# Kernel optimization log

Hardware: AMD Instinct MI355X
Metric: run time of the kernel (lower is better)

The kernel has to match this reference:

```python
import jax, jax.numpy as jnp
import numpy as np

B, NW = 1024, 300
N = NW // 3          # 100 tokens (keypoints)
E = 5                # token dim after cat of PE(2): 3 + 2
H, D, L = 4, 64, 3   # heads, d_attention, layers


def setup_inputs() -> dict:
    key = jax.random.key(0)
    ks = jax.random.split(key, 8)
    s = jnp.float32(0.1)
    x = jax.random.normal(ks[0], (B, NW), dtype=jnp.float32)
    Wq = jax.random.normal(ks[1], (L, H, D, E), dtype=jnp.float32) * s  # per-head W_Q (no bias)
    Wk = jax.random.normal(ks[2], (L, H, D, E), dtype=jnp.float32) * s
    Wv = jax.random.normal(ks[3], (L, H, D, E), dtype=jnp.float32) * s
    Wo = jax.random.normal(ks[4], (L, E, H * D), dtype=jnp.float32) * s  # MHA output proj (no bias)
    Wf = jax.random.normal(ks[5], (L, E, E), dtype=jnp.float32) * s      # FFN linear
    bf = jax.random.normal(ks[6], (L, E), dtype=jnp.float32) * s
    g1 = jnp.ones((L, E), dtype=jnp.float32)
    b1 = jnp.zeros((L, E), dtype=jnp.float32)
    g2 = jnp.ones((L, E), dtype=jnp.float32)
    b2 = jnp.zeros((L, E), dtype=jnp.float32)
    return dict(x=x, Wq=Wq, Wk=Wk, Wv=Wv, Wo=Wo, Wf=Wf, bf=bf,
                g1=g1, b1=b1, g2=g2, b2=b2)


def _layer_norm(x, g, b, eps=1e-5):
    mu = jnp.mean(x, axis=-1, keepdims=True)
    var = jnp.mean((x - mu) ** 2, axis=-1, keepdims=True)  # biased, like torch LN
    return (x - mu) / jnp.sqrt(var + eps) * g + b


def reference(x, Wq, Wk, Wv, Wo, Wf, bf, g1, b1, g2, b2):
    kp = x.reshape(B, N, 3)                      # 'b (n d) -> b n d', d=3
    mask = kp[:, :, -1] > 0                      # [B,N] keypoint confidence mask
    # PositionalEncoding(d_model=2, kind='cat'): div_term=[1] -> pe=[sin(pos),cos(pos)]
    pos = jnp.arange(N, dtype=jnp.float32)
    pe = jnp.stack([jnp.sin(pos), jnp.cos(pos)], axis=-1)         # [N,2]
    out = jnp.concatenate([kp, jnp.broadcast_to(pe, (B, N, 2))], axis=-1)  # [B,N,5]
    out = jnp.where(mask[:, :, None], out, jnp.float32(0.0))      # out[~mask]=0

    pair = mask[:, None, None, :] & mask[:, None, :, None]        # [B,1,N,N]
    neg = -jnp.finfo(jnp.float32).max
    scale = jnp.float32(1.0 / np.sqrt(D))
    for l in range(L):
        # per-head projections (heads vectorized over h)
        q = jnp.einsum('bne,hde->bhnd', out, Wq[l])
        k = jnp.einsum('bne,hde->bhnd', out, Wk[l])
        v = jnp.einsum('bne,hde->bhnd', out, Wv[l])
        dots = jnp.einsum('bhid,bhjd->bhij', q, k) * scale        # [B,H,N,N]
        dots = jnp.where(pair, dots, neg)
        attn = jax.nn.softmax(dots, axis=-1)
        o = jnp.einsum('bhij,bhjd->bhid', attn, v)                # [B,H,N,D]
        o = o.transpose(0, 2, 1, 3).reshape(B, N, H * D)          # concat heads
        attn_out = o @ Wo[l].T                                    # [B,N,E]
        ln1 = _layer_norm(attn_out + out, g1[l], b1[l])
        ffn = jax.nn.relu(ln1 @ Wf[l].T + bf[l])
        out = _layer_norm(ffn + ln1, g2[l], b2[l])
    return out
```

## Files before the change

### kernel.cpp

```cpp
#include <hip/hip_runtime.h>
#include <math.h>

#define NTOK 100
#define EDIM 5
#define NH   4
#define NL   3
#define DD   64
#define BLK  256

__global__ void precompute_mp(const float* __restrict__ Wq,
                              const float* __restrict__ Wk,
                              const float* __restrict__ Wv,
                              const float* __restrict__ Wo,
                              float* __restrict__ mp) {
  const int blk = blockIdx.x;
  const int which = blk / 12;
  const int rem = blk % 12;
  const int l = rem / 4, h = rem % 4;
  const int t = threadIdx.x;

  __shared__ float A[320];
  __shared__ float Bsh[320];

  const float* wa = (which ? Wv : Wq) + (l*NH + h)*DD*EDIM;
  for (int r = t; r < 320; r += 64) A[r] = wa[r];
  if (which == 0) {
    const float* wk = Wk + (l*NH + h)*DD*EDIM;
    for (int r = t; r < 320; r += 64) Bsh[r] = wk[r];
  } else {
    for (int r = t; r < 320; r += 64) {
      int f = r >> 6, d = r & 63;
      Bsh[r] = Wo[(l*EDIM + f)*(NH*DD) + h*DD + d];
    }
  }
  __syncthreads();
  if (t < 25) {
    int e = t / 5, f = t % 5;
    float acc = 0.f;
    if (which == 0) {
      #pragma unroll 8
      for (int d = 0; d < DD; ++d) acc += A[d*5+e] * Bsh[d*5+f];
      acc *= 0.125f * 1.44269504088896340736f;
    } else {
      #pragma unroll 8
      for (int d = 0; d < DD; ++d) acc += A[d*5+e] * Bsh[f*64+d];
    }
    mp[which*960 + ((l*NH + h)*EDIM + e)*8 + f] = acc;
  }
}

__global__ __launch_bounds__(BLK, 4) void encoder_kernel(
    const float* __restrict__ x,
    const float* __restrict__ mp,
    const float* __restrict__ Wf,
    const float* __restrict__ bfv,
    const float* __restrict__ g1,
    const float* __restrict__ b1,
    const float* __restrict__ g2,
    const float* __restrict__ b2,
    float* __restrict__ out)
{
  const int b = blockIdx.x, t = threadIdx.x;
  const int wv = t >> 6;
  const int ln = t & 63;

  __shared__ float4 s_MP4[480];
  __shared__ float4 s_o4[NH][NTOK+2];
  __shared__ float  s_o1[NH][NTOK+2];
  __shared__ float4 s_wp4[2][NH][NTOK+2];
  __shared__ float  s_wp1[2][NH][NTOK+2];
  __shared__ int    s_cidx[NTOK];
  __shared__ unsigned long long s_bal[2];

  const float* mpf = (const float*)s_MP4;
  for (int r = t; r < 480; r += BLK) s_MP4[r] = ((const float4*)mp)[r];

  float k0=0.f, k1=0.f, k2=0.f, msk=0.f;
  if (t < NTOK) {
    k0 = x[b*300 + 3*t];
    k1 = x[b*300 + 3*t + 1];
    k2 = x[b*300 + 3*t + 2];
    msk = (k2 > 0.f) ? 1.f : 0.f;
  }
  unsigned long long bal = __ballot(t < NTOK && msk != 0.f);
  if (t == 0)  s_bal[0] = bal;
  if (t == 64) s_bal[1] = bal;
  __syncthreads();
  const unsigned long long bw0 = s_bal[0], bw1 = s_bal[1];
  const int nm = __popcll(bw0) + __popcll(bw1);
  if (t < NTOK) {
    int lane = t & 63;
    unsigned long long lm = (lane == 0) ? 0ull : ((1ull << lane) - 1ull);
    int pre = (t < 64) ? __popcll(bw0 & lm) : (__popcll(bw0) + __popcll(bw1 & lm));
    if (msk != 0.f) {
      float4 v = make_float4(k0, k1, k2, sinf((float)t));
      float v4 = cosf((float)t);
      #pragma unroll
      for (int w = 0; w < NH; ++w) { s_o4[w][pre] = v; s_o1[w][pre] = v4; }
      s_cidx[t] = pre;
    } else {
      s_cidx[t] = nm;
    }
  }
  if (t == 0) {
    #pragma unroll
    for (int w = 0; w < NH; ++w) {
      s_o4[w][nm] = make_float4(0.f,0.f,0.f,0.f);
      s_o1[w][nm] = 0.f;
    }
  }
  __syncthreads();

  const int rows = nm + 1;
  const int npass = (rows > 64) ? 2 : 1;
  const float4* ow4 = s_o4[wv];
  const float*  ow1 = s_o1[wv];
  int bufp = 0;

  for (int l = 0; l < NL; ++l) {
    const float* Mh = mpf + ((l*NH + wv)*EDIM)*8;
    const float* Ph = mpf + 960 + ((l*NH + wv)*EDIM)*8;

    for (int ps = 0; ps < npass; ++ps) {
      const int i = ln + (ps << 6);
      if (i < rows) {
        const bool rep = (i == nm);
        float4 ov = ow4[i]; float ov4 = ow1[i];
        float o_[5] = {ov.x, ov.y, ov.z, ov.w, ov4};
        float a0=0.f,a1=0.f,a2=0.f,a3=0.f,a4=0.f;
        #pragma unroll
        for (int e = 0; e < 5; ++e) {
          float4 mr = *(const float4*)(Mh + e*8); float m4 = Mh[e*8+4];
          a0 += o_[e]*mr.x; a1 += o_[e]*mr.y; a2 += o_[e]*mr.z;
          a3 += o_[e]*mr.w; a4 += o_[e]*m4;
        }
        if (rep) { a0=0.f; a1=0.f; a2=0.f; a3=0.f; a4=0.f; }

        float w0=0.f,w1=0.f,w2=0.f,w3=0.f,w4=0.f, ls=0.f;
        #pragma unroll 4
        for (int j = 0; j < nm; ++j) {
          float4 oj = ow4[j]; float oe = ow1[j];
          float s = a0*oj.x + a1*oj.y + a2*oj.z + a3*oj.w + a4*oe;
          float p = exp2f(s);
          ls += p;
          w0 += p*oj.x; w1 += p*oj.y; w2 += p*oj.z; w3 += p*oj.w; w4 += p*oe;
        }
        if (rep) {
          float wext = (float)(NTOK - nm);
          w0 += wext*o_[0]; w1 += wext*o_[1]; w2 += wext*o_[2];
          w3 += wext*o_[3]; w4 += wext*o_[4];
        }
        float inv = 1.f / (rep ? (float)NTOK : ls);
        float we[5] = {w0,w1,w2,w3,w4};
        float c0=0.f,c1=0.f,c2=0.f,c3=0.f,c4=0.f;
        #pragma unroll
        for (int e = 0; e < 5; ++e) {
          float4 pr = *(const float4*)(Ph + e*8); float p4 = Ph[e*8+4];
          c0 += we[e]*pr.x; c1 += we[e]*pr.y; c2 += we[e]*pr.z;
          c3 += we[e]*pr.w; c4 += we[e]*p4;
        }
        s_wp4[bufp][wv][i] = make_float4(c0*inv, c1*inv, c2*inv, c3*inv);
        s_wp1[bufp][wv][i] = c4*inv;
      }
    }
    __syncthreads();

    for (int ps = 0; ps < npass; ++ps) {
      const int i = ln + (ps << 6);
      if (i < rows) {
        float4 ov = ow4[i]; float ov4 = ow1[i];
        float y[5] = {ov.x, ov.y, ov.z, ov.w, ov4};
        #pragma unroll
        for (int hh = 0; hh < NH; ++hh) {
          float4 wa = s_wp4[bufp][hh][i];
          y[0] += wa.x; y[1] += wa.y; y[2] += wa.z; y[3] += wa.w;
          y[4] += s_wp1[bufp][hh][i];
        }
        float mu = 0.2f*(y[0]+y[1]+y[2]+y[3]+y[4]);
        float var = 0.f;
        #pragma unroll
        for (int e = 0; e < 5; ++e) { float d = y[e]-mu; var += d*d; }
        var *= 0.2f;
        float inv1 = 1.f / sqrtf(var + 1e-5f);
        float ln1[5];
        #pragma unroll
        for (int e = 0; e < 5; ++e) ln1[e] = (y[e]-mu)*inv1*g1[l*5+e] + b1[l*5+e];
        float r2[5];
        #pragma unroll
        for (int e = 0; e < 5; ++e) {
          float acc = bfv[l*5+e];
          #pragma unroll
          for (int f = 0; f < 5; ++f) acc += ln1[f]*Wf[(l*5+e)*5+f];
          acc = acc > 0.f ? acc : 0.f;
          r2[e] = acc + ln1[e];
        }
        float mu2 = 0.2f*(r2[0]+r2[1]+r2[2]+r2[3]+r2[4]);
        float var2 = 0.f;
        #pragma unroll
        for (int e = 0; e < 5; ++e) { float d = r2[e]-mu2; var2 += d*d; }
        var2 *= 0.2f;
        float inv2 = 1.f / sqrtf(var2 + 1e-5f);
        float no[5];
        #pragma unroll
        for (int e = 0; e < 5; ++e) no[e] = (r2[e]-mu2)*inv2*g2[l*5+e] + b2[l*5+e];
        s_o4[wv][i] = make_float4(no[0], no[1], no[2], no[3]);
        s_o1[wv][i] = no[4];
      }
    }
    bufp ^= 1;
  }
  __syncthreads();

  for (int r = t; r < NTOK*EDIM; r += BLK) {
    int i = r / EDIM;
    int e = r - i*EDIM;
    int c = s_cidx[i];
    float v = (e < 4) ? ((const float*)&s_o4[0][c])[e] : s_o1[0][c];
    out[b*(NTOK*EDIM) + r] = v;
  }
}

extern "C" void kernel_launch(void* const* d_in, const int* in_sizes, int n_in,
                              void* d_out, int out_size, void* d_ws, size_t ws_size,
                              hipStream_t stream) {
  const float* x  = (const float*)d_in[0];
  const float* Wq = (const float*)d_in[1];
  const float* Wk = (const float*)d_in[2];
  const float* Wv = (const float*)d_in[3];
  const float* Wo = (const float*)d_in[4];
  const float* Wf = (const float*)d_in[5];
  const float* bf = (const float*)d_in[6];
  const float* g1 = (const float*)d_in[7];
  const float* b1 = (const float*)d_in[8];
  const float* g2 = (const float*)d_in[9];
  const float* b2 = (const float*)d_in[10];
  float* outp = (float*)d_out;
  float* mp   = (float*)d_ws;

  precompute_mp<<<24, 64, 0, stream>>>(Wq, Wk, Wv, Wo, mp);
  encoder_kernel<<<1024, BLK, 0, stream>>>(x, mp, Wf, bf, g1, b1, g2, b2, outp);
}
```

Measured before the change: 138.9 us.

## Split key range across two waves per head and broadcast keys via readlane

Doubles the block to 512 threads so that each head gets two waves, and each wave handles half of the compacted key range. The partial exp-sums and weighted sums are merged in the update phase. Token states now stay in registers, and keys are broadcast with readlane instead of being re-read from shared memory per head. The change also uses the hardware exp2 and rcp intrinsics. It is meant to cut the serial per-lane key loop length and LDS traffic, at the cost of more threads per block, higher register pressure and an extra shared merge.

```diff
diff --git a/kernel.cpp b/kernel.cpp
--- a/kernel.cpp
+++ b/kernel.cpp
@@ -6,7 +6,19 @@
 #define NH   4
 #define NL   3
 #define DD   64
-#define BLK  256
+#define BLK  512
+
+#if __has_builtin(__builtin_amdgcn_exp2f)
+#define EXP2(x) __builtin_amdgcn_exp2f(x)
+#else
+#define EXP2(x) exp2f(x)
+#endif
+#if __has_builtin(__builtin_amdgcn_rcpf)
+#define RCPF(x) __builtin_amdgcn_rcpf(x)
+#else
+#define RCPF(x) (1.f/(x))
+#endif
+#define RL(v, l) __int_as_float(__builtin_amdgcn_readlane(__float_as_int(v), (l)))
 
 __global__ void precompute_mp(const float* __restrict__ Wq,
                               const float* __restrict__ Wk,
@@ -49,7 +61,7 @@
   }
 }
 
-__global__ __launch_bounds__(BLK, 4) void encoder_kernel(
+__global__ __launch_bounds__(BLK, 8) void encoder_kernel(
     const float* __restrict__ x,
     const float* __restrict__ mp,
     const float* __restrict__ Wf,
@@ -61,19 +73,20 @@
     float* __restrict__ out)
 {
   const int b = blockIdx.x, t = threadIdx.x;
-  const int wv = t >> 6;
-  const int ln = t & 63;
+  const int wv = t >> 6, ln = t & 63;
+  const int h = wv >> 1, g = wv & 1;
 
   __shared__ float4 s_MP4[480];
-  __shared__ float4 s_o4[NH][NTOK+2];
-  __shared__ float  s_o1[NH][NTOK+2];
-  __shared__ float4 s_wp4[2][NH][NTOK+2];
-  __shared__ float  s_wp1[2][NH][NTOK+2];
+  __shared__ float4 s_w4[NH][2][104];
+  __shared__ float2 s_w2[NH][2][104];
+  __shared__ float4 s_i4[104];
+  __shared__ float  s_i1[104];
   __shared__ int    s_cidx[NTOK];
   __shared__ unsigned long long s_bal[2];
 
   const float* mpf = (const float*)s_MP4;
   for (int r = t; r < 480; r += BLK) s_MP4[r] = ((const float4*)mp)[r];
+  for (int r = t; r < 104; r += BLK) { s_i4[r] = make_float4(0.f,0.f,0.f,0.f); s_i1[r] = 0.f; }
 
   float k0=0.f, k1=0.f, k2=0.f, msk=0.f;
   if (t < NTOK) {
@@ -93,129 +106,148 @@
     unsigned long long lm = (lane == 0) ? 0ull : ((1ull << lane) - 1ull);
     int pre = (t < 64) ? __popcll(bw0 & lm) : (__popcll(bw0) + __popcll(bw1 & lm));
     if (msk != 0.f) {
-      float4 v = make_float4(k0, k1, k2, sinf((float)t));
-      float v4 = cosf((float)t);
-      #pragma unroll
-      for (int w = 0; w < NH; ++w) { s_o4[w][pre] = v; s_o1[w][pre] = v4; }
+      s_i4[pre] = make_float4(k0, k1, k2, sinf((float)t));
+      s_i1[pre] = cosf((float)t);
       s_cidx[t] = pre;
     } else {
       s_cidx[t] = nm;
     }
   }
-  if (t == 0) {
-    #pragma unroll
-    for (int w = 0; w < NH; ++w) {
-      s_o4[w][nm] = make_float4(0.f,0.f,0.f,0.f);
-      s_o1[w][nm] = 0.f;
-    }
-  }
   __syncthreads();
 
   const int rows = nm + 1;
-  const int npass = (rows > 64) ? 2 : 1;
-  const float4* ow4 = s_o4[wv];
-  const float*  ow1 = s_o1[wv];
-  int bufp = 0;
+  const bool twoRows = (rows > 64);
+
+  float oA0,oA1,oA2,oA3,oA4, oB0,oB1,oB2,oB3,oB4;
+  { float4 v = s_i4[ln]; oA0=v.x; oA1=v.y; oA2=v.z; oA3=v.w; oA4=s_i1[ln]; }
+  if (ln < 40) { float4 v = s_i4[ln+64]; oB0=v.x; oB1=v.y; oB2=v.z; oB3=v.w; oB4=s_i1[ln+64]; }
+  else { oB0=0.f; oB1=0.f; oB2=0.f; oB3=0.f; oB4=0.f; }
+
+  const int jmid = nm >> 1;
+  const int jlo  = g ? jmid : 0;
+  const int jhi  = g ? nm : jmid;
+  const int jhiA = (jhi < 64) ? jhi : 64;
+  const int jloB = (jlo > 64) ? jlo : 64;
+  const float wext = (float)(NTOK - nm);
 
   for (int l = 0; l < NL; ++l) {
-    const float* Mh = mpf + ((l*NH + wv)*EDIM)*8;
-    const float* Ph = mpf + 960 + ((l*NH + wv)*EDIM)*8;
-
-    for (int ps = 0; ps < npass; ++ps) {
-      const int i = ln + (ps << 6);
-      if (i < rows) {
-        const bool rep = (i == nm);
-        float4 ov = ow4[i]; float ov4 = ow1[i];
-        float o_[5] = {ov.x, ov.y, ov.z, ov.w, ov4};
-        float a0=0.f,a1=0.f,a2=0.f,a3=0.f,a4=0.f;
+    const float* Mh = mpf + ((l*NH + h)*EDIM)*8;
+    const float* Ph = mpf + 960 + ((l*NH + h)*EDIM)*8;
+
+    auto attn_row = [&](float o0,float o1,float o2,float o3,float o4,int row) {
+      float oc[5] = {o0,o1,o2,o3,o4};
+      float a0=0.f,a1=0.f,a2=0.f,a3=0.f,a4=0.f;
+      #pragma unroll
+      for (int e = 0; e < 5; ++e) {
+        float4 mr = *(const float4*)(Mh + e*8); float m4 = Mh[e*8+4];
+        a0 += oc[e]*mr.x; a1 += oc[e]*mr.y; a2 += oc[e]*mr.z;
+        a3 += oc[e]*mr.w; a4 += oc[e]*m4;
+      }
+      const bool rep = (row == nm);
+      if (rep) { a0=0.f; a1=0.f; a2=0.f; a3=0.f; a4=0.f; }
+      float ls=0.f, w0=0.f, w1=0.f, w2=0.f, w3=0.f, w4=0.f;
+      #pragma unroll 4
+      for (int j = jlo; j < jhiA; ++j) {
+        float ox = RL(oA0,j), oy = RL(oA1,j), oz = RL(oA2,j),
+              ow = RL(oA3,j), oe = RL(oA4,j);
+        float s = a0*ox + a1*oy + a2*oz + a3*ow + a4*oe;
+        float p = EXP2(s);
+        ls += p;
+        w0 += p*ox; w1 += p*oy; w2 += p*oz; w3 += p*ow; w4 += p*oe;
+      }
+      #pragma unroll 4
+      for (int j = jloB; j < jhi; ++j) {
+        int jl = j - 64;
+        float ox = RL(oB0,jl), oy = RL(oB1,jl), oz = RL(oB2,jl),
+              ow = RL(oB3,jl), oe = RL(oB4,jl);
+        float s = a0*ox + a1*oy + a2*oz + a3*ow + a4*oe;
+        float p = EXP2(s);
+        ls += p;
+        w0 += p*ox; w1 += p*oy; w2 += p*oz; w3 += p*ow; w4 += p*oe;
+      }
+      if (rep && g == 0) {
+        w0 += wext*o0; w1 += wext*o1; w2 += wext*o2; w3 += wext*o3; w4 += wext*o4;
+      }
+      float wc[5] = {w0,w1,w2,w3,w4};
+      float c0=0.f,c1=0.f,c2=0.f,c3=0.f,c4=0.f;
+      #pragma unroll
+      for (int e = 0; e < 5; ++e) {
+        float4 pr = *(const float4*)(Ph + e*8); float p4 = Ph[e*8+4];
+        c0 += wc[e]*pr.x; c1 += wc[e]*pr.y; c2 += wc[e]*pr.z;
+        c3 += wc[e]*pr.w; c4 += wc[e]*p4;
+      }
+      if (row < rows) {
+        s_w4[h][g][row] = make_float4(c0,c1,c2,c3);
+        s_w2[h][g][row] = make_float2(c4, ls);
+      }
+    };
+
+    attn_row(oA0,oA1,oA2,oA3,oA4, ln);
+    if (twoRows) attn_row(oB0,oB1,oB2,oB3,oB4, ln+64);
+    __syncthreads();
+
+    auto upd = [&](float& p0,float& p1,float& p2,float& p3,float& p4,int row) {
+      if (row >= rows) return;
+      const bool rep = (row == nm);
+      float y0=p0, y1=p1, y2=p2, y3=p3, y4=p4;
+      #pragma unroll
+      for (int hh = 0; hh < NH; ++hh) {
+        float4 wA = s_w4[hh][0][row], wB = s_w4[hh][1][row];
+        float2 lA = s_w2[hh][0][row], lB = s_w2[hh][1][row];
+        float ls  = lA.y + lB.y;
+        float inv = rep ? 0.01f : RCPF(ls);
+        y0 += (wA.x + wB.x)*inv; y1 += (wA.y + wB.y)*inv;
+        y2 += (wA.z + wB.z)*inv; y3 += (wA.w + wB.w)*inv;
+        y4 += (lA.x + lB.x)*inv;
+      }
+      float yv[5] = {y0,y1,y2,y3,y4};
+      float mu = 0.2f*(y0+y1+y2+y3+y4);
+      float var = 0.f;
+      #pragma unroll
+      for (int e = 0; e < 5; ++e) { float d = yv[e]-mu; var += d*d; }
+      var *= 0.2f;
+      float iv = 1.f / sqrtf(var + 1e-5f);
+      float l1[5];
+      #pragma unroll
+      for (int e = 0; e < 5; ++e) l1[e] = (yv[e]-mu)*iv*g1[l*5+e] + b1[l*5+e];
+      float r2[5];
+      #pragma unroll
+      for (int e = 0; e < 5; ++e) {
+        float acc = bfv[l*5+e];
         #pragma unroll
-        for (int e = 0; e < 5; ++e) {
-          float4 mr = *(const float4*)(Mh + e*8); float m4 = Mh[e*8+4];
-          a0 += o_[e]*mr.x; a1 += o_[e]*mr.y; a2 += o_[e]*mr.z;
-          a3 += o_[e]*mr.w; a4 += o_[e]*m4;
-        }
-        if (rep) { a0=0.f; a1=0.f; a2=0.f; a3=0.f; a4=0.f; }
-
-        float w0=0.f,w1=0.f,w2=0.f,w3=0.f,w4=0.f, ls=0.f;
-        #pragma unroll 4
-        for (int j = 0; j < nm; ++j) {
-          float4 oj = ow4[j]; float oe = ow1[j];
-          float s = a0*oj.x + a1*oj.y + a2*oj.z + a3*oj.w + a4*oe;
-          float p = exp2f(s);
-          ls += p;
-          w0 += p*oj.x; w1 += p*oj.y; w2 += p*oj.z; w3 += p*oj.w; w4 += p*oe;
-        }
-        if (rep) {
-          float wext = (float)(NTOK - nm);
-          w0 += wext*o_[0]; w1 += wext*o_[1]; w2 += wext*o_[2];
-          w3 += wext*o_[3]; w4 += wext*o_[4];
-        }
-        float inv = 1.f / (rep ? (float)NTOK : ls);
-        float we[5] = {w0,w1,w2,w3,w4};
-        float c0=0.f,c1=0.f,c2=0.f,c3=0.f,c4=0.f;
-        #pragma unroll
-        for (int e = 0; e < 5; ++e) {
-          float4 pr = *(const float4*)(Ph + e*8); float p4 = Ph[e*8+4];
-          c0 += we[e]*pr.x; c1 += we[e]*pr.y; c2 += we[e]*pr.z;
-          c3 += we[e]*pr.w; c4 += we[e]*p4;
-        }
-        s_wp4[bufp][wv][i] = make_float4(c0*inv, c1*inv, c2*inv, c3*inv);
-        s_wp1[bufp][wv][i] = c4*inv;
-      }
-    }
+        for (int f = 0; f < 5; ++f) acc += l1[f]*Wf[(l*5+e)*5+f];
+        acc = acc > 0.f ? acc : 0.f;
+        r2[e] = acc + l1[e];
+      }
+      float mu2 = 0.2f*(r2[0]+r2[1]+r2[2]+r2[3]+r2[4]);
+      float var2 = 0.f;
+      #pragma unroll
+      for (int e = 0; e < 5; ++e) { float d = r2[e]-mu2; var2 += d*d; }
+      var2 *= 0.2f;
+      float iv2 = 1.f / sqrtf(var2 + 1e-5f);
+      p0 = (r2[0]-mu2)*iv2*g2[l*5+0] + b2[l*5+0];
+      p1 = (r2[1]-mu2)*iv2*g2[l*5+1] + b2[l*5+1];
+      p2 = (r2[2]-mu2)*iv2*g2[l*5+2] + b2[l*5+2];
+      p3 = (r2[3]-mu2)*iv2*g2[l*5+3] + b2[l*5+3];
+      p4 = (r2[4]-mu2)*iv2*g2[l*5+4] + b2[l*5+4];
+    };
+    upd(oA0,oA1,oA2,oA3,oA4, ln);
+    if (twoRows) upd(oB0,oB1,oB2,oB3,oB4, ln+64);
     __syncthreads();
-
-    for (int ps = 0; ps < npass; ++ps) {
-      const int i = ln + (ps << 6);
-      if (i < rows) {
-        float4 ov = ow4[i]; float ov4 = ow1[i];
-        float y[5] = {ov.x, ov.y, ov.z, ov.w, ov4};
-        #pragma unroll
-        for (int hh = 0; hh < NH; ++hh) {
-          float4 wa = s_wp4[bufp][hh][i];
-          y[0] += wa.x; y[1] += wa.y; y[2] += wa.z; y[3] += wa.w;
-          y[4] += s_wp1[bufp][hh][i];
-        }
-        float mu = 0.2f*(y[0]+y[1]+y[2]+y[3]+y[4]);
-        float var = 0.f;
-        #pragma unroll
-        for (int e = 0; e < 5; ++e) { float d = y[e]-mu; var += d*d; }
-        var *= 0.2f;
-        float inv1 = 1.f / sqrtf(var + 1e-5f);
-        float ln1[5];
-        #pragma unroll
-        for (int e = 0; e < 5; ++e) ln1[e] = (y[e]-mu)*inv1*g1[l*5+e] + b1[l*5+e];
-        float r2[5];
-        #pragma unroll
-        for (int e = 0; e < 5; ++e) {
-          float acc = bfv[l*5+e];
-          #pragma unroll
-          for (int f = 0; f < 5; ++f) acc += ln1[f]*Wf[(l*5+e)*5+f];
-          acc = acc > 0.f ? acc : 0.f;
-          r2[e] = acc + ln1[e];
-        }
-        float mu2 = 0.2f*(r2[0]+r2[1]+r2[2]+r2[3]+r2[4]);
-        float var2 = 0.f;
-        #pragma unroll
-        for (int e = 0; e < 5; ++e) { float d = r2[e]-mu2; var2 += d*d; }
-        var2 *= 0.2f;
-        float inv2 = 1.f / sqrtf(var2 + 1e-5f);
-        float no[5];
-        #pragma unroll
-        for (int e = 0; e < 5; ++e) no[e] = (r2[e]-mu2)*inv2*g2[l*5+e] + b2[l*5+e];
-        s_o4[wv][i] = make_float4(no[0], no[1], no[2], no[3]);
-        s_o1[wv][i] = no[4];
-      }
-    }
-    bufp ^= 1;
-  }
-  __syncthreads();
-
+  }
+
+  if (wv == 0) {
+    if (ln < rows) { s_i4[ln] = make_float4(oA0,oA1,oA2,oA3); s_i1[ln] = oA4; }
+    if (twoRows && (ln + 64 < rows)) {
+      s_i4[ln+64] = make_float4(oB0,oB1,oB2,oB3); s_i1[ln+64] = oB4;
+    }
+  }
+  __syncthreads();
   for (int r = t; r < NTOK*EDIM; r += BLK) {
     int i = r / EDIM;
     int e = r - i*EDIM;
     int c = s_cidx[i];
-    float v = (e < 4) ? ((const float*)&s_o4[0][c])[e] : s_o1[0][c];
+    float v = (e < 4) ? ((const float*)&s_i4[c])[e] : s_i1[c];
     out[b*(NTOK*EDIM) + r] = v;
   }
 }
```

New measurement: 146.6 us. +5.5%, slower.
